# Optimization experiments

Hardware: AMD Instinct MI355X
Metric: run time of the kernel (lower is better)

The kernel has to match this reference:

```python
import jax, jax.numpy as jnp
import numpy as np

B, N, D = 16, 1024, 768
MU = 768
R = 16
DR = D // R  # 48


def _dyn_linear(x, mu, Wg, bg, Bg, bb, in_f, out_f):
    """DynamicLinear: per-sample weights generated from mu via a hypernetwork.
    Wg: [MU, out_f*in_f], bg: [out_f*in_f], Bg: [MU, out_f], bb: [out_f].
    x: [B, in_f] or [B, N, in_f].
    """
    Bsz = mu.shape[0]
    W = (mu @ Wg + bg).reshape(Bsz, out_f, in_f)  # [B, out, in]
    b = mu @ Bg + bb                              # [B, out]
    if x.ndim == 2:
        return jnp.einsum('bi,boi->bo', x, W) + b
    return jnp.einsum('bni,boi->bno', x, W) + b[:, None, :]


def setup_inputs() -> dict:
    key = jax.random.key(0)
    ks = jax.random.split(key, 12)
    s = 0.02
    return {
        'x': jax.random.normal(ks[0], (B, N, D), jnp.float32),
        'mu': jax.random.normal(ks[1], (B, MU), jnp.float32),
        # ChannelGate MLP layer 1: D -> D//R
        'Wg1': jax.random.normal(ks[2], (MU, DR * D), jnp.float32) * s,
        'bg1': jnp.zeros((DR * D,), jnp.float32),
        'Bg1': jax.random.normal(ks[3], (MU, DR), jnp.float32) * s,
        'bb1': jnp.zeros((DR,), jnp.float32),
        # ChannelGate MLP layer 2: D//R -> D
        'Wg2': jax.random.normal(ks[4], (MU, D * DR), jnp.float32) * s,
        'bg2': jnp.zeros((D * DR,), jnp.float32),
        'Bg2': jax.random.normal(ks[5], (MU, D), jnp.float32) * s,
        'bb2': jnp.zeros((D,), jnp.float32),
        # SpatialGate: D -> 1
        'Wgs': jax.random.normal(ks[6], (MU, D), jnp.float32) * s,
        'bgs': jnp.zeros((D,), jnp.float32),
        'Bgs': jax.random.normal(ks[7], (MU, 1), jnp.float32) * s,
        'bbs': jnp.zeros((1,), jnp.float32),
    }


def reference(x, mu, Wg1, bg1, Bg1, bb1, Wg2, bg2, Bg2, bb2, Wgs, bgs, Bgs, bbs):
    def mlp(p):  # p: [B, D]
        h = jax.nn.relu(_dyn_linear(p, mu, Wg1, bg1, Bg1, bb1, D, DR))
        return _dyn_linear(h, mu, Wg2, bg2, Bg2, bb2, DR, D)

    # ChannelGate: avg + max pooling over token dim, shared dynamic MLP
    avg_pool = jnp.mean(x, axis=1)          # [B, D]
    max_pool = jnp.max(x, axis=1)           # [B, D]
    channel_att = mlp(avg_pool) + mlp(max_pool)
    x = x * jax.nn.sigmoid(channel_att)[:, None, :]

    # SpatialGate: per-token dynamic scalar gate
    s = _dyn_linear(x, mu, Wgs, bgs, Bgs, bbs, D, 1)  # [B, N, 1]
    return x * jax.nn.sigmoid(s)
```

## Files before the change

kernel.cpp:

```cpp
#include <hip/hip_runtime.h>
#include <math.h>


#define B_  16
#define N_  1024
#define D_  768
#define MU_ 768

__global__ __launch_bounds__(192) void k_pool(
    const float* __restrict__ x, const float* __restrict__ mu,
    float* __restrict__ mu_t, float* __restrict__ psum, float* __restrict__ pmax)
{
    int blk = blockIdx.x;
    if (blk == 512) {
        for (int e = threadIdx.x; e < MU_ * B_; e += 192) {
            int m = e >> 4, b = e & 15;
            mu_t[e] = mu[b * MU_ + m];
        }
        return;
    }
    int b = blk >> 5, c = blk & 31;
    int d4 = threadIdx.x << 2;
    const float* xp = x + ((size_t)(b * N_ + c * 32)) * D_ + d4;
    float s0 = 0.f, s1 = 0.f, s2 = 0.f, s3 = 0.f;
    float m0 = -3.4e38f, m1 = -3.4e38f, m2 = -3.4e38f, m3 = -3.4e38f;
    for (int n = 0; n < 32; ++n) {
        float4 v = *(const float4*)(xp + (size_t)n * D_);
        s0 += v.x; s1 += v.y; s2 += v.z; s3 += v.w;
        m0 = fmaxf(m0, v.x); m1 = fmaxf(m1, v.y);
        m2 = fmaxf(m2, v.z); m3 = fmaxf(m3, v.w);
    }
    size_t o = ((size_t)(c * B_ + b)) * D_ + d4;
    float4 sv = { s0, s1, s2, s3 }; *(float4*)(psum + o) = sv;
    float4 mv = { m0, m1, m2, m3 }; *(float4*)(pmax + o) = mv;
}

__global__ __launch_bounds__(256) void k_hyper(
    const float* __restrict__ Wg1, const float* __restrict__ Wg2,
    const float* __restrict__ Wgs, const float* __restrict__ Bg2,
    const float* __restrict__ mu_t,
    float* __restrict__ w1p, float* __restrict__ w2p,
    float* __restrict__ wsp, float* __restrict__ b2p)
{
    int t = blockIdx.x, tid = threadIdx.x;

    const float* mat; float* outp; int ncols, h, colbase;
    if (t < 576) {
        int mi = t >= 288; int tt0 = t - (mi ? 288 : 0);
        h = tt0 / 144; int tile = tt0 % 144;
        mat = mi ? Wg2 : Wg1;
        outp = (mi ? w2p : w1p) + (size_t)h * 589824;
        ncols = 36864; colbase = tile << 8;
    } else if (t < 582) {
        int u = t - 576; h = u / 3; int tile = u % 3;
        mat = Wgs; outp = wsp + (size_t)h * 12288; ncols = 768; colbase = tile << 8;
    } else {
        int u = t - 582; h = u / 3; int tile = u % 3;
        mat = Bg2; outp = b2p + (size_t)h * 12288; ncols = 768; colbase = tile << 8;
    }
    int m0 = h * 384;

    int ct = tid & 63;
    int bqu = __builtin_amdgcn_readfirstlane(tid >> 6);
    const float* p   = mat + (size_t)m0 * ncols + colbase + (ct << 2);
    const float* mus = mu_t + (size_t)m0 * 16 + (bqu << 2);

    float4 acc[4];
    #pragma unroll
    for (int i = 0; i < 4; ++i) acc[i] = make_float4(0.f, 0.f, 0.f, 0.f);

    for (int mt = 0; mt < 48; ++mt) {
        float4 wv[8];
        #pragma unroll
        for (int u = 0; u < 8; ++u)
            wv[u] = *(const float4*)(p + (size_t)u * ncols);
        p += (size_t)8 * ncols;
        #pragma unroll
        for (int u = 0; u < 8; ++u) {
            float4 mv = *(const float4*)(mus + (((mt << 3) + u) << 4));
            acc[0].x = fmaf(mv.x, wv[u].x, acc[0].x);
            acc[0].y = fmaf(mv.x, wv[u].y, acc[0].y);
            acc[0].z = fmaf(mv.x, wv[u].z, acc[0].z);
            acc[0].w = fmaf(mv.x, wv[u].w, acc[0].w);
            acc[1].x = fmaf(mv.y, wv[u].x, acc[1].x);
            acc[1].y = fmaf(mv.y, wv[u].y, acc[1].y);
            acc[1].z = fmaf(mv.y, wv[u].z, acc[1].z);
            acc[1].w = fmaf(mv.y, wv[u].w, acc[1].w);
            acc[2].x = fmaf(mv.z, wv[u].x, acc[2].x);
            acc[2].y = fmaf(mv.z, wv[u].y, acc[2].y);
            acc[2].z = fmaf(mv.z, wv[u].z, acc[2].z);
            acc[2].w = fmaf(mv.z, wv[u].w, acc[2].w);
            acc[3].x = fmaf(mv.w, wv[u].x, acc[3].x);
            acc[3].y = fmaf(mv.w, wv[u].y, acc[3].y);
            acc[3].z = fmaf(mv.w, wv[u].z, acc[3].z);
            acc[3].w = fmaf(mv.w, wv[u].w, acc[3].w);
        }
    }

    #pragma unroll
    for (int i = 0; i < 4; ++i)
        *(float4*)(outp + (size_t)((bqu << 2) + i) * ncols + colbase + (ct << 2)) = acc[i];
}

__global__ __launch_bounds__(256) void k_redW(
    const float* __restrict__ w1p, const float* __restrict__ w2p,
    const float* __restrict__ wsp, const float* __restrict__ b2p,
    const float* __restrict__ bg1, const float* __restrict__ bg2,
    const float* __restrict__ bgs, const float* __restrict__ bb2,
    float* __restrict__ w1, float* __restrict__ w2,
    float* __restrict__ wsw, float* __restrict__ b2v)
{
    int i4 = blockIdx.x * 256 + threadIdx.x;
    const float* src; const float* bias; float* dst; int loc, bcols4;
    if (i4 < 147456)       { src = w1p; bias = bg1; dst = w1;  loc = i4;          bcols4 = 9216; }
    else if (i4 < 294912)  { src = w2p; bias = bg2; dst = w2;  loc = i4 - 147456; bcols4 = 9216; }
    else if (i4 < 297984)  { src = wsp; bias = bgs; dst = wsw; loc = i4 - 294912; bcols4 = 192; }
    else                   { src = b2p; bias = bb2; dst = b2v; loc = i4 - 297984; bcols4 = 192; }
    int half_stride4 = bcols4 * 16;
    float4 a = ((const float4*)src)[loc];
    float4 b = ((const float4*)src)[loc + half_stride4];
    float4 bi = ((const float4*)bias)[loc % bcols4];
    float4 o = { a.x + b.x + bi.x, a.y + b.y + bi.y,
                 a.z + b.z + bi.z, a.w + b.w + bi.w };
    ((float4*)dst)[loc] = o;
}

__global__ __launch_bounds__(128) void k_red(
    const float* __restrict__ psum, const float* __restrict__ pmax,
    const float* __restrict__ mu, const float* __restrict__ Bgs,
    const float* __restrict__ bbs,
    float* __restrict__ avgb, float* __restrict__ maxb, float* __restrict__ bs)
{
    int b = blockIdx.x / 6, tile = blockIdx.x % 6, tid = threadIdx.x;
    int d = tile * 128 + tid;
    float s = 0.f, mx = -3.4e38f;
    for (int c = 0; c < 32; ++c) {
        size_t idx = ((size_t)(c * B_ + b)) * D_ + d;
        s += psum[idx];
        mx = fmaxf(mx, pmax[idx]);
    }
    avgb[b * D_ + d] = s * (1.f / 1024.f);
    maxb[b * D_ + d] = mx;

    if (tile == 0) {
        __shared__ float sb[128];
        float p = 0.f;
        for (int m = tid; m < MU_; m += 128) p += mu[b * MU_ + m] * Bgs[m];
        sb[tid] = p;
        __syncthreads();
        if (tid < 64) {
            float v = sb[tid] + sb[tid + 64];
            #pragma unroll
            for (int k = 32; k; k >>= 1) v += __shfl_xor(v, k, 64);
            if (tid == 0) bs[b] = v + bbs[0];
        }
    }
}

__global__ __launch_bounds__(64) void k_c1(
    const float* __restrict__ w1, const float* __restrict__ avgb,
    const float* __restrict__ maxb, const float* __restrict__ mu,
    const float* __restrict__ Bg1, const float* __restrict__ bb1,
    float* __restrict__ g)
{
    int b = blockIdx.x / 48, o = blockIdx.x % 48, ln = threadIdx.x;
    const float* row = w1 + (size_t)b * 36864 + o * 768;
    const float* av  = avgb + b * D_;
    const float* mxp = maxb + b * D_;
    const float* mub = mu + b * MU_;
    float pa = 0.f, pm = 0.f, pb = 0.f;
    #pragma unroll
    for (int i = 0; i < 12; ++i) {
        int idx = ln + (i << 6);
        float wv = row[idx];
        pa += wv * av[idx];
        pm += wv * mxp[idx];
        pb += Bg1[(size_t)idx * 48 + o] * mub[idx];
    }
    #pragma unroll
    for (int k = 32; k; k >>= 1) {
        pa += __shfl_xor(pa, k, 64);
        pm += __shfl_xor(pm, k, 64);
        pb += __shfl_xor(pb, k, 64);
    }
    if (ln == 0) {
        float bb = pb + bb1[o];
        g[b * 48 + o] = fmaxf(pa + bb, 0.f) + fmaxf(pm + bb, 0.f);
    }
}

__global__ __launch_bounds__(64) void k_c2(
    const float* __restrict__ w2, const float* __restrict__ b2w,
    const float* __restrict__ g, float* __restrict__ cg)
{
    __shared__ float gL[48];
    int b = blockIdx.x / 12, tile = blockIdx.x % 12, ln = threadIdx.x;
    if (ln < 48) gL[ln] = g[b * 48 + ln];
    __syncthreads();
    int d = (tile << 6) + ln;
    const float* row = w2 + (size_t)b * 36864 + d * 48;
    float att = 0.f;
    #pragma unroll
    for (int o = 0; o < 48; o += 4) {
        float4 w4 = *(const float4*)(row + o);
        att += w4.x * gL[o] + w4.y * gL[o + 1] + w4.z * gL[o + 2] + w4.w * gL[o + 3];
    }
    att += 2.f * b2w[b * D_ + d];
    cg[b * D_ + d] = 1.f / (1.f + expf(-att));
}

__global__ __launch_bounds__(256) void k_final(
    const float* __restrict__ x, const float* __restrict__ cg,
    const float* __restrict__ wsw, const float* __restrict__ bs,
    float* __restrict__ out)
{
    int wv = threadIdx.x >> 6, ln = threadIdx.x & 63;
    int tok = (blockIdx.x << 2) + wv;
    int b = tok >> 10;
    const float* xp = x + (size_t)tok * D_;
    const float* cp = cg + b * D_;
    const float* wp = wsw + b * D_;
    float xg[12];
    float part = 0.f;
    #pragma unroll
    for (int q = 0; q < 3; ++q) {
        int d = (q << 8) + (ln << 2);
        float4 xv = *(const float4*)(xp + d);
        float4 cv = *(const float4*)(cp + d);
        float4 w4 = *(const float4*)(wp + d);
        float g0 = xv.x * cv.x, g1 = xv.y * cv.y;
        float g2 = xv.z * cv.z, g3 = xv.w * cv.w;
        part += g0 * w4.x + g1 * w4.y + g2 * w4.z + g3 * w4.w;
        xg[q * 4 + 0] = g0; xg[q * 4 + 1] = g1;
        xg[q * 4 + 2] = g2; xg[q * 4 + 3] = g3;
    }
    #pragma unroll
    for (int k = 32; k; k >>= 1) part += __shfl_xor(part, k, 64);
    float s = part + bs[b];
    float sig = 1.f / (1.f + expf(-s));
    #pragma unroll
    for (int q = 0; q < 3; ++q) {
        int d = (q << 8) + (ln << 2);
        float4 o4 = { xg[q * 4 + 0] * sig, xg[q * 4 + 1] * sig,
                      xg[q * 4 + 2] * sig, xg[q * 4 + 3] * sig };
        *(float4*)(out + (size_t)tok * D_ + d) = o4;
    }
}

extern "C" void kernel_launch(void* const* d_in, const int* in_sizes, int n_in,
                              void* d_out, int out_size, void* d_ws, size_t ws_size,
                              hipStream_t stream)
{
    const float* x   = (const float*)d_in[0];
    const float* mu  = (const float*)d_in[1];
    const float* Wg1 = (const float*)d_in[2];
    const float* bg1 = (const float*)d_in[3];
    const float* Bg1 = (const float*)d_in[4];
    const float* bb1 = (const float*)d_in[5];
    const float* Wg2 = (const float*)d_in[6];
    const float* bg2 = (const float*)d_in[7];
    const float* Bg2 = (const float*)d_in[8];
    const float* bb2 = (const float*)d_in[9];
    const float* Wgs = (const float*)d_in[10];
    const float* bgs = (const float*)d_in[11];
    const float* Bgs = (const float*)d_in[12];
    const float* bbs = (const float*)d_in[13];
    float* base = (float*)d_ws;
    float* out  = (float*)d_out;

    float* mu_t = base;
    float* psum = mu_t + 12288;
    float* pmax = psum + 393216;
    float* w1p  = pmax + 393216;
    float* w2p  = w1p  + 1179648;
    float* wsp  = w2p  + 1179648;
    float* b2p  = wsp  + 24576;
    float* w1   = b2p  + 24576;
    float* w2   = w1   + 589824;
    float* wsw  = w2   + 589824;
    float* b2v  = wsw  + 12288;
    float* avgb = b2v  + 12288;
    float* maxb = avgb + 12288;
    float* g    = maxb + 12288;
    float* bs   = g    + 768;
    float* cg   = bs   + 16;

    hipLaunchKernelGGL(k_pool,  dim3(513),  dim3(192), 0, stream, x, mu, mu_t, psum, pmax);
    hipLaunchKernelGGL(k_hyper, dim3(588),  dim3(256), 0, stream,
                       Wg1, Wg2, Wgs, Bg2, mu_t, w1p, w2p, wsp, b2p);
    hipLaunchKernelGGL(k_redW,  dim3(1176), dim3(256), 0, stream,
                       w1p, w2p, wsp, b2p, bg1, bg2, bgs, bb2, w1, w2, wsw, b2v);
    hipLaunchKernelGGL(k_red,   dim3(96),   dim3(128), 0, stream,
                       psum, pmax, mu, Bgs, bbs, avgb, maxb, bs);
    hipLaunchKernelGGL(k_c1,    dim3(768),  dim3(64),  0, stream,
                       w1, avgb, maxb, mu, Bg1, bb1, g);
    hipLaunchKernelGGL(k_c2,    dim3(192),  dim3(64),  0, stream, w2, b2v, g, cg);
    hipLaunchKernelGGL(k_final, dim3(4096), dim3(256), 0, stream, x, cg, wsw, bs, out);
}
```

Before: 129.6 us.

## Retile hypernetwork GEMM to all 16 samples per thread with 4-way K split

The hypernetwork kernel now has each thread compute all 16 batch rows for one float4 of columns, over a quarter of the MU dimension. Each weight float4 is therefore read once and reused 16 times, where before four waves each reloaded it for 4 samples, and the K split grows from 2 to 4 slices. The partial-sum reduction now adds four slices plus bias and writes the result in place, which removes the separate reduced-weight buffers. The cost is a 64-register accumulator per thread, which raises register pressure and lowers occupancy. The partial-sum buffers double in size, so the reduction kernel reads more data.

After: 175.4 us. 35.3% more time.

```diff
diff --git a/kernel.cpp b/kernel.cpp
--- a/kernel.cpp
+++ b/kernel.cpp
@@ -35,7 +35,25 @@
     float4 mv = { m0, m1, m2, m3 }; *(float4*)(pmax + o) = mv;
 }
 
-__global__ __launch_bounds__(256) void k_hyper(
+#define HFMA(MB, A0, A1, A2, A3) \
+    acc[A0].x = fmaf(MB.x, wv.x, acc[A0].x); \
+    acc[A0].y = fmaf(MB.x, wv.y, acc[A0].y); \
+    acc[A0].z = fmaf(MB.x, wv.z, acc[A0].z); \
+    acc[A0].w = fmaf(MB.x, wv.w, acc[A0].w); \
+    acc[A1].x = fmaf(MB.y, wv.x, acc[A1].x); \
+    acc[A1].y = fmaf(MB.y, wv.y, acc[A1].y); \
+    acc[A1].z = fmaf(MB.y, wv.z, acc[A1].z); \
+    acc[A1].w = fmaf(MB.y, wv.w, acc[A1].w); \
+    acc[A2].x = fmaf(MB.z, wv.x, acc[A2].x); \
+    acc[A2].y = fmaf(MB.z, wv.y, acc[A2].y); \
+    acc[A2].z = fmaf(MB.z, wv.z, acc[A2].z); \
+    acc[A2].w = fmaf(MB.z, wv.w, acc[A2].w); \
+    acc[A3].x = fmaf(MB.w, wv.x, acc[A3].x); \
+    acc[A3].y = fmaf(MB.w, wv.y, acc[A3].y); \
+    acc[A3].z = fmaf(MB.w, wv.z, acc[A3].z); \
+    acc[A3].w = fmaf(MB.w, wv.w, acc[A3].w);
+
+__global__ __launch_bounds__(256, 2) void k_hyper(
     const float* __restrict__ Wg1, const float* __restrict__ Wg2,
     const float* __restrict__ Wgs, const float* __restrict__ Bg2,
     const float* __restrict__ mu_t,
@@ -43,86 +61,71 @@
     float* __restrict__ wsp, float* __restrict__ b2p)
 {
     int t = blockIdx.x, tid = threadIdx.x;
+    int w = tid >> 6, ln = tid & 63;
 
     const float* mat; float* outp; int ncols, h, colbase;
-    if (t < 576) {
-        int mi = t >= 288; int tt0 = t - (mi ? 288 : 0);
-        h = tt0 / 144; int tile = tt0 % 144;
+    if (t < 288) {
+        int mi = t / 144; int r = t % 144;
+        h = r / 36; int chunk = r % 36;
         mat = mi ? Wg2 : Wg1;
-        outp = (mi ? w2p : w1p) + (size_t)h * 589824;
-        ncols = 36864; colbase = tile << 8;
-    } else if (t < 582) {
-        int u = t - 576; h = u / 3; int tile = u % 3;
-        mat = Wgs; outp = wsp + (size_t)h * 12288; ncols = 768; colbase = tile << 8;
+        outp = mi ? w2p : w1p;
+        ncols = 36864; colbase = chunk << 10;
+    } else if (t < 292) {
+        h = t - 288; mat = Wgs; outp = wsp; ncols = 768; colbase = 0;
+        if (w == 3) return;
     } else {
-        int u = t - 582; h = u / 3; int tile = u % 3;
-        mat = Bg2; outp = b2p + (size_t)h * 12288; ncols = 768; colbase = tile << 8;
-    }
-    int m0 = h * 384;
-
-    int ct = tid & 63;
-    int bqu = __builtin_amdgcn_readfirstlane(tid >> 6);
-    const float* p   = mat + (size_t)m0 * ncols + colbase + (ct << 2);
-    const float* mus = mu_t + (size_t)m0 * 16 + (bqu << 2);
-
-    float4 acc[4];
-    #pragma unroll
-    for (int i = 0; i < 4; ++i) acc[i] = make_float4(0.f, 0.f, 0.f, 0.f);
-
-    for (int mt = 0; mt < 48; ++mt) {
-        float4 wv[8];
-        #pragma unroll
-        for (int u = 0; u < 8; ++u)
-            wv[u] = *(const float4*)(p + (size_t)u * ncols);
-        p += (size_t)8 * ncols;
-        #pragma unroll
-        for (int u = 0; u < 8; ++u) {
-            float4 mv = *(const float4*)(mus + (((mt << 3) + u) << 4));
-            acc[0].x = fmaf(mv.x, wv[u].x, acc[0].x);
-            acc[0].y = fmaf(mv.x, wv[u].y, acc[0].y);
-            acc[0].z = fmaf(mv.x, wv[u].z, acc[0].z);
-            acc[0].w = fmaf(mv.x, wv[u].w, acc[0].w);
-            acc[1].x = fmaf(mv.y, wv[u].x, acc[1].x);
-            acc[1].y = fmaf(mv.y, wv[u].y, acc[1].y);
-            acc[1].z = fmaf(mv.y, wv[u].z, acc[1].z);
-            acc[1].w = fmaf(mv.y, wv[u].w, acc[1].w);
-            acc[2].x = fmaf(mv.z, wv[u].x, acc[2].x);
-            acc[2].y = fmaf(mv.z, wv[u].y, acc[2].y);
-            acc[2].z = fmaf(mv.z, wv[u].z, acc[2].z);
-            acc[2].w = fmaf(mv.z, wv[u].w, acc[2].w);
-            acc[3].x = fmaf(mv.w, wv[u].x, acc[3].x);
-            acc[3].y = fmaf(mv.w, wv[u].y, acc[3].y);
-            acc[3].z = fmaf(mv.w, wv[u].z, acc[3].z);
-            acc[3].w = fmaf(mv.w, wv[u].w, acc[3].w);
-        }
-    }
-
-    #pragma unroll
-    for (int i = 0; i < 4; ++i)
-        *(float4*)(outp + (size_t)((bqu << 2) + i) * ncols + colbase + (ct << 2)) = acc[i];
+        h = t - 292; mat = Bg2; outp = b2p; ncols = 768; colbase = 0;
+        if (w == 3) return;
+    }
+    int m0 = h * 192;
+    int col = colbase + (w << 8) + (ln << 2);
+    const float* p   = mat + (size_t)m0 * ncols + col;
+    const float* mus = mu_t + (m0 << 4);
+
+    float4 acc[16];
+    #pragma unroll
+    for (int i = 0; i < 16; ++i) acc[i] = make_float4(0.f, 0.f, 0.f, 0.f);
+
+    #pragma unroll 4
+    for (int m = 0; m < 192; ++m) {
+        float4 wv = *(const float4*)p; p += ncols;
+        const float4* mr = (const float4*)(mus + (m << 4));
+        float4 u0 = mr[0], u1 = mr[1], u2 = mr[2], u3 = mr[3];
+        HFMA(u0, 0, 1, 2, 3)
+        HFMA(u1, 4, 5, 6, 7)
+        HFMA(u2, 8, 9, 10, 11)
+        HFMA(u3, 12, 13, 14, 15)
+    }
+
+    float* op = outp + (size_t)(h << 4) * ncols + col;
+    #pragma unroll
+    for (int b = 0; b < 16; ++b)
+        *(float4*)(op + (size_t)b * ncols) = acc[b];
 }
 
 __global__ __launch_bounds__(256) void k_redW(
-    const float* __restrict__ w1p, const float* __restrict__ w2p,
-    const float* __restrict__ wsp, const float* __restrict__ b2p,
+    float* __restrict__ w1p, float* __restrict__ w2p,
+    float* __restrict__ wsp, float* __restrict__ b2p,
     const float* __restrict__ bg1, const float* __restrict__ bg2,
-    const float* __restrict__ bgs, const float* __restrict__ bb2,
-    float* __restrict__ w1, float* __restrict__ w2,
-    float* __restrict__ wsw, float* __restrict__ b2v)
+    const float* __restrict__ bgs, const float* __restrict__ bb2)
 {
     int i4 = blockIdx.x * 256 + threadIdx.x;
-    const float* src; const float* bias; float* dst; int loc, bcols4;
-    if (i4 < 147456)       { src = w1p; bias = bg1; dst = w1;  loc = i4;          bcols4 = 9216; }
-    else if (i4 < 294912)  { src = w2p; bias = bg2; dst = w2;  loc = i4 - 147456; bcols4 = 9216; }
-    else if (i4 < 297984)  { src = wsp; bias = bgs; dst = wsw; loc = i4 - 294912; bcols4 = 192; }
-    else                   { src = b2p; bias = bb2; dst = b2v; loc = i4 - 297984; bcols4 = 192; }
-    int half_stride4 = bcols4 * 16;
-    float4 a = ((const float4*)src)[loc];
-    float4 b = ((const float4*)src)[loc + half_stride4];
+    float* arr; const float* bias; int loc, bcols4;
+    if (i4 < 147456)       { arr = w1p; bias = bg1; loc = i4;          bcols4 = 9216; }
+    else if (i4 < 294912)  { arr = w2p; bias = bg2; loc = i4 - 147456; bcols4 = 9216; }
+    else if (i4 < 297984)  { arr = wsp; bias = bgs; loc = i4 - 294912; bcols4 = 192; }
+    else                   { arr = b2p; bias = bb2; loc = i4 - 297984; bcols4 = 192; }
+    int qstride = bcols4 * 16;
+    float4 a0 = ((const float4*)arr)[loc];
+    float4 a1 = ((const float4*)arr)[loc + qstride];
+    float4 a2 = ((const float4*)arr)[loc + 2 * qstride];
+    float4 a3 = ((const float4*)arr)[loc + 3 * qstride];
     float4 bi = ((const float4*)bias)[loc % bcols4];
-    float4 o = { a.x + b.x + bi.x, a.y + b.y + bi.y,
-                 a.z + b.z + bi.z, a.w + b.w + bi.w };
-    ((float4*)dst)[loc] = o;
+    float4 o = { a0.x + a1.x + a2.x + a3.x + bi.x,
+                 a0.y + a1.y + a2.y + a3.y + bi.y,
+                 a0.z + a1.z + a2.z + a3.z + bi.z,
+                 a0.w + a1.w + a2.w + a3.w + bi.w };
+    ((float4*)arr)[loc] = o;
 }
 
 __global__ __launch_bounds__(128) void k_red(
@@ -272,28 +275,24 @@
     float* psum = mu_t + 12288;
     float* pmax = psum + 393216;
     float* w1p  = pmax + 393216;
-    float* w2p  = w1p  + 1179648;
-    float* wsp  = w2p  + 1179648;
-    float* b2p  = wsp  + 24576;
-    float* w1   = b2p  + 24576;
-    float* w2   = w1   + 589824;
-    float* wsw  = w2   + 589824;
-    float* b2v  = wsw  + 12288;
-    float* avgb = b2v  + 12288;
+    float* w2p  = w1p  + 2359296;
+    float* wsp  = w2p  + 2359296;
+    float* b2p  = wsp  + 49152;
+    float* avgb = b2p  + 49152;
     float* maxb = avgb + 12288;
     float* g    = maxb + 12288;
     float* bs   = g    + 768;
     float* cg   = bs   + 16;
 
     hipLaunchKernelGGL(k_pool,  dim3(513),  dim3(192), 0, stream, x, mu, mu_t, psum, pmax);
-    hipLaunchKernelGGL(k_hyper, dim3(588),  dim3(256), 0, stream,
+    hipLaunchKernelGGL(k_hyper, dim3(296),  dim3(256), 0, stream,
                        Wg1, Wg2, Wgs, Bg2, mu_t, w1p, w2p, wsp, b2p);
     hipLaunchKernelGGL(k_redW,  dim3(1176), dim3(256), 0, stream,
-                       w1p, w2p, wsp, b2p, bg1, bg2, bgs, bb2, w1, w2, wsw, b2v);
+                       w1p, w2p, wsp, b2p, bg1, bg2, bgs, bb2);
     hipLaunchKernelGGL(k_red,   dim3(96),   dim3(128), 0, stream,
                        psum, pmax, mu, Bgs, bbs, avgb, maxb, bs);
     hipLaunchKernelGGL(k_c1,    dim3(768),  dim3(64),  0, stream,
-                       w1, avgb, maxb, mu, Bg1, bb1, g);
-    hipLaunchKernelGGL(k_c2,    dim3(192),  dim3(64),  0, stream, w2, b2v, g, cg);
-    hipLaunchKernelGGL(k_final, dim3(4096), dim3(256), 0, stream, x, cg, wsw, bs, out);
-}
+                       w1p, avgb, maxb, mu, Bg1, bb1, g);
+    hipLaunchKernelGGL(k_c2,    dim3(192),  dim3(64),  0, stream, w2p, b2p, g, cg);
+    hipLaunchKernelGGL(k_final, dim3(4096), dim3(256), 0, stream, x, cg, wsp, bs, out);
+}
```
